# Kernel tuning notes

Hardware: AMD Instinct MI355X
Metric: run time of the kernel (lower is better)

## Reference

```python
import jax, jax.numpy as jnp
import numpy as np

EPS = 1e-06
SOUND_SPEED = 343.0
SUBBAND_EDGES = [500.0, 2000.0, 8000.0]
IS_SOUND_IDX = 0
RHO_IDX = 1
NUM_CANDIDATES = 64


def setup_inputs() -> dict:
    key = jax.random.key(0)
    ks = jax.random.split(key, 6)
    B, T, F, S, D = 16, 2048, 1025, 4, NUM_CANDIDATES
    phase = jax.random.normal(ks[0], (B, 1, T, F), dtype=jnp.float32)
    comb = jax.random.normal(ks[1], (B, 2, T, F), dtype=jnp.float32)
    scalar = jax.random.normal(ks[2], (B, T, S), dtype=jnp.float32)
    scalar_observed_mask = jax.random.uniform(ks[3], (B, T, S), dtype=jnp.float32)
    scalar_reliable_mask = jax.random.uniform(ks[4], (B, T, S), dtype=jnp.float32)
    stpacc = jax.random.normal(ks[5], (B, 1, T, D), dtype=jnp.float32)
    # STFT bin centers up to 24 kHz
    frequencies_hz = (jnp.arange(F, dtype=jnp.float32) * (24000.0 / (F - 1)))
    spacing_grid_hz = jnp.linspace(50.0, 1000.0, D, dtype=jnp.float32)
    return {
        'phase': phase, 'comb': comb, 'scalar': scalar,
        'scalar_observed_mask': scalar_observed_mask,
        'scalar_reliable_mask': scalar_reliable_mask,
        'stpacc': stpacc, 'frequencies_hz': frequencies_hz,
        'spacing_grid_hz': spacing_grid_hz,
    }


def _periodicity_basis(freq, spacing):
    # [D, F]: raised-cosine comb pattern for each candidate spacing
    pattern = 0.5 * (1.0 + jnp.cos(2.0 * np.pi * (freq[None, :] / jnp.maximum(spacing[:, None], 1e-06))))
    return pattern / jnp.maximum(pattern.mean(axis=-1, keepdims=True), EPS)


def _subband_masks(freq):
    # static boundaries: [min(f)] + edges + [max(f)+1]; all bands nonempty for this grid
    bounds = [jnp.min(freq)] + [jnp.float32(e) for e in SUBBAND_EDGES] + [jnp.max(freq) + 1.0]
    masks = [((freq >= lo) & (freq < hi)).astype(freq.dtype) for lo, hi in zip(bounds[:-1], bounds[1:])]
    return jnp.stack(masks, axis=0)  # [S_band, F]


def reference(phase, comb, scalar, scalar_observed_mask, scalar_reliable_mask,
              stpacc, frequencies_hz, spacing_grid_hz):
    freq = frequencies_hz.astype(phase.dtype)
    log_mag = phase[:, 0, :, :]                 # [B,T,F]
    smooth_d1 = comb[:, 0, :, :]
    abs_d1 = jnp.abs(comb[:, 1, :, :])
    log_mag_centered = log_mag - jnp.mean(log_mag, axis=-1, keepdims=True)
    trough = jax.nn.relu(-log_mag_centered)
    d1_strength = jax.nn.relu(abs_d1) + 0.25 * jax.nn.relu(jnp.abs(smooth_d1))
    trough = trough * (1.0 + d1_strength)
    trough = trough / jnp.maximum(jnp.mean(trough, axis=-1, keepdims=True), EPS)

    basis = _periodicity_basis(freq, spacing_grid_hz.astype(phase.dtype))  # [D,F]
    D, F = basis.shape
    periodic_score = jnp.einsum('btf,df->btd', trough, basis) / float(F)

    channels = [periodic_score]
    bands = _subband_masks(freq)                           # [Sb,F]
    denom = jnp.maximum(jnp.sum(bands, axis=-1), 1.0)      # [Sb]
    masked_basis = basis[None, :, :] * bands[:, None, :]   # [Sb,D,F]
    band_scores = jnp.einsum('btf,sdf->bstd', trough, masked_basis) / denom[None, :, None, None]
    channels += [band_scores[:, s] for s in range(bands.shape[0])]

    # stpacc projection (last dim already == D, no interpolation needed)
    stp = jax.nn.relu(stpacc[:, 0, :, :])
    stp = stp / jnp.maximum(jnp.mean(stp, axis=-1, keepdims=True), EPS)
    channels.append(stp)

    B, T = trough.shape[0], trough.shape[1]
    obs_quality = jnp.broadcast_to(jnp.mean(scalar_observed_mask, axis=-1, keepdims=True), (B, T, D))
    rel_quality = jnp.broadcast_to(jnp.mean(scalar_reliable_mask, axis=-1, keepdims=True), (B, T, D))
    channels.append(obs_quality)
    channels.append(rel_quality)

    is_sound = jnp.broadcast_to(jnp.clip(scalar[:, :, IS_SOUND_IDX:IS_SOUND_IDX + 1], 0.0, 1.0), (B, T, D))
    channels.append(is_sound)
    rho = jnp.broadcast_to(jnp.abs(jnp.clip(scalar[:, :, RHO_IDX:RHO_IDX + 1], -1.0, 1.0)), (B, T, D))
    channels.append(rho)

    raw_likelihood_seq = jnp.stack(channels, axis=-1)      # [B,T,D,10]
    raw_distance_logits_seq = jnp.mean(raw_likelihood_seq, axis=-1) * (0.5 + 0.5 * is_sound)

    distance_grid_cm = (100.0 * SOUND_SPEED) / (2.0 * jnp.maximum(spacing_grid_hz, 1e-06))
    return (raw_likelihood_seq, raw_distance_logits_seq,
            spacing_grid_hz.astype(phase.dtype), distance_grid_cm.astype(phase.dtype))
```

## Files before the change

### kernel.cpp

```cpp
#include <hip/hip_runtime.h>
#include <hip/hip_fp16.h>
#include <math.h>

#define Bn 16
#define Tn 2048
#define Fn 1025
#define KP 1056
#define KROW 1064
#define ROWS 16
#define NSLOT 11
#define Dn 64
#define EPSF 1e-6f

typedef __attribute__((ext_vector_type(8))) _Float16 f16x8;
typedef __attribute__((ext_vector_type(4))) _Float16 f16x4;
typedef __attribute__((ext_vector_type(4))) float f32x4;

__device__ inline float waveReduceSum(float v) {
#pragma unroll
  for (int off = 32; off > 0; off >>= 1) v += __shfl_xor(v, off, 64);
  return v;
}

__global__ __launch_bounds__(256) void prep_kernel(
    const float* __restrict__ freq, const float* __restrict__ spacing,
    _Float16* __restrict__ basisT, float* __restrict__ out2, float* __restrict__ out3) {
  __shared__ float wsum[4];
  const int d = blockIdx.x;
  const int tid = threadIdx.x;
  const float sp = fmaxf(spacing[d], 1e-6f);

  float pv[5];
  float lsum = 0.f;
#pragma unroll
  for (int it = 0; it < 5; ++it) {
    int f = tid + 256 * it;
    float p = 0.f;
    if (f < Fn) {
      double arg = 6.2831853071795864769 * (double)(freq[f] / sp);
      p = 0.5f * (1.0f + (float)cos(arg));
      lsum += p;
    }
    pv[it] = p;
  }
  float s = waveReduceSum(lsum);
  if ((tid & 63) == 0) wsum[tid >> 6] = s;
  __syncthreads();
  float inv = 1.0f / fmaxf((wsum[0] + wsum[1] + wsum[2] + wsum[3]) * (1.0f / 1025.0f), EPSF);

#pragma unroll
  for (int it = 0; it < 5; ++it) {
    int f = tid + 256 * it;
    if (f < KP) basisT[(size_t)d * KP + f] = (_Float16)(pv[it] * inv);
  }
  if (tid == 0) {
    out2[d] = spacing[d];
    out3[d] = 17150.0f / sp;
  }
}

__global__ __launch_bounds__(1024) void fused_kernel(
    const float* __restrict__ phase, const float* __restrict__ comb,
    const _Float16* __restrict__ basisT,
    const float* __restrict__ scalar, const float* __restrict__ obs_m,
    const float* __restrict__ rel_m, const float* __restrict__ stpacc,
    float* __restrict__ out0, float* __restrict__ out1) {
  __shared__ _Float16 uLDS[ROWS * KROW];
  __shared__ float cumS[ROWS * NSLOT * 65];
  __shared__ float rowScale[ROWS];

  const int lane = threadIdx.x & 63;
  const int w = __builtin_amdgcn_readfirstlane(threadIdx.x >> 6);
  const int row0 = blockIdx.x * ROWS;

  {
    const int row = row0 + w;
    const int b = row >> 11;
    const int t = row & 2047;
    const float* prow  = phase + (size_t)row * Fn;
    const float* c0row = comb + ((size_t)(b * 2 + 0) * Tn + t) * Fn;
    const float* c1row = comb + ((size_t)(b * 2 + 1) * Tn + t) * Fn;

    float4 pv[5], c0v[5], c1v[5];
#pragma unroll
    for (int it = 0; it < 5; ++it) {
      const int i = lane + 64 * it;
      if (i < 256) {
        pv[it]  = *(const float4*)(prow  + 4 * i);
        c0v[it] = *(const float4*)(c0row + 4 * i);
        c1v[it] = *(const float4*)(c1row + 4 * i);
      } else if (i == 256) {
        pv[it]  = make_float4(prow[1024],  0.f, 0.f, 0.f);
        c0v[it] = make_float4(c0row[1024], 0.f, 0.f, 0.f);
        c1v[it] = make_float4(c1row[1024], 0.f, 0.f, 0.f);
      } else {
        pv[it]  = make_float4(0.f, 0.f, 0.f, 0.f);
        c0v[it] = make_float4(0.f, 0.f, 0.f, 0.f);
        c1v[it] = make_float4(0.f, 0.f, 0.f, 0.f);
      }
    }

    float s = 0.f;
#pragma unroll
    for (int it = 0; it < 5; ++it)
      s += pv[it].x + pv[it].y + pv[it].z + pv[it].w;
    s = waveReduceSum(s);
    const float mean_lm = s * (1.0f / 1025.0f);

    _Float16* urow = uLDS + (size_t)w * KROW;
    float su = 0.f;
#pragma unroll
    for (int it = 0; it < 5; ++it) {
      const int i = lane + 64 * it;
      float4 u;
      const float* pf = (const float*)&pv[it];
      const float* q0 = (const float*)&c0v[it];
      const float* q1 = (const float*)&c1v[it];
      float* uf = (float*)&u;
#pragma unroll
      for (int c2 = 0; c2 < 4; ++c2) {
        float tr = fmaxf(mean_lm - pf[c2], 0.f);
        float d1 = fabsf(q1[c2]) + 0.25f * fabsf(q0[c2]);
        uf[c2] = tr * (1.f + d1);
      }
      if (i > 256) { u.x = 0.f; u.y = 0.f; u.z = 0.f; u.w = 0.f; }
      else if (i == 256) { u.y = 0.f; u.z = 0.f; u.w = 0.f; }
      su += u.x + u.y + u.z + u.w;
      if (i < 264) {
        f16x4 hv;
#pragma unroll
        for (int c2 = 0; c2 < 4; ++c2) hv[c2] = (_Float16)uf[c2];
        *(f16x4*)(urow + 4 * i) = hv;
      }
    }
    su = waveReduceSum(su);
    if (lane == 0) rowScale[w] = 1.0f / fmaxf(su * (1.0f / 1025.0f), EPSF);
  }
  __syncthreads();

  const int m16 = lane & 15;
  const int kg = lane >> 4;
  const int nh = w & 1;
  const int kh = w >> 1;
  const int d0 = nh * 32 + m16;

  const _Float16* ALp = uLDS + (size_t)m16 * KROW + kg * 8;
  const _Float16* B0 = basisT + (size_t)d0 * KP + kg * 8;
  const _Float16* B1 = basisT + (size_t)(d0 + 16) * KP + kg * 8;

  f32x4 acc0 = {0.f, 0.f, 0.f, 0.f};
  f32x4 acc1 = {0.f, 0.f, 0.f, 0.f};

  auto loadA = [&](int kt) { return *(const f16x8*)(ALp + kt * 32); };
  auto tileA = [&](int kt, f16x8 a) {
    f16x8 b0 = *(const f16x8*)(B0 + kt * 32);
    f16x8 b1 = *(const f16x8*)(B1 + kt * 32);
    acc0 = __builtin_amdgcn_mfma_f32_16x16x32_f16(a, b0, acc0, 0, 0, 0);
    acc1 = __builtin_amdgcn_mfma_f32_16x16x32_f16(a, b1, acc1, 0, 0, 0);
  };
  auto stor = [&](int slot, const f32x4& v0, const f32x4& v1) {
#pragma unroll
    for (int r = 0; r < 4; ++r) {
      const int rr = kg * 4 + r;
      cumS[(rr * NSLOT + slot) * 65 + d0]      = v0[r];
      cumS[(rr * NSLOT + slot) * 65 + d0 + 16] = v1[r];
    }
  };
  auto boundary = [&](int kt, int KB, f32x4& sa, f32x4& sb) {
    f16x8 a = loadA(kt);
    const int kb = kt * 32 + kg * 8;
    f16x8 alo, ahi;
#pragma unroll
    for (int j = 0; j < 8; ++j) {
      bool lo = (kb + j) < KB;
      alo[j] = lo ? a[j] : (_Float16)0.f;
      ahi[j] = lo ? (_Float16)0.f : a[j];
    }
    tileA(kt, alo);
    sa = acc0; sb = acc1;
    tileA(kt, ahi);
  };

  if (kh == 0) {
    f32x4 s0a = acc0, s0b = acc0, s1a = acc0, s1b = acc0;
    boundary(0, 22, s0a, s0b);
    tileA(1, loadA(1));
    boundary(2, 86, s1a, s1b);
    tileA(3, loadA(3));
    stor(0, acc0, acc1);
    stor(8, s0a, s0b);
    stor(9, s1a, s1b);
  } else if (kh == 2) {
    f32x4 s2a = acc0, s2b = acc0;
    tileA(8, loadA(8));
    tileA(9, loadA(9));
    boundary(10, 342, s2a, s2b);
    tileA(11, loadA(11));
    stor(2, acc0, acc1);
    stor(10, s2a, s2b);
  } else {
    const int kb = kh * 4;
    const int ke = (kh == 7) ? 33 : kb + 4;
#pragma unroll 4
    for (int kt = kb; kt < ke; ++kt) tileA(kt, loadA(kt));
    stor(kh, acc0, acc1);
  }
  __syncthreads();

  {
    const int rl = w;
    const size_t bt = (size_t)(row0 + rl);
    const float rs = rowScale[rl];

    float sv = fmaxf(stpacc[bt * Dn + lane], 0.f);

    float q[NSLOT];
#pragma unroll
    for (int s2 = 0; s2 < NSLOT; ++s2)
      q[s2] = cumS[(rl * NSLOT + s2) * 65 + lane];

    float total = q[0] + q[1] + q[2] + q[3] + q[4] + q[5] + q[6] + q[7];
    float cum342 = q[0] + q[1] + q[10];

    float ssum = waveReduceSum(sv);
    float stp = sv / fmaxf(ssum * (1.0f / 64.0f), EPSF);

    float4 scv = *(const float4*)(scalar + bt * 4);
    float4 om  = *(const float4*)(obs_m  + bt * 4);
    float4 rm  = *(const float4*)(rel_m  + bt * 4);
    float obs_q = (om.x + om.y + om.z + om.w) * 0.25f;
    float rel_q = (rm.x + rm.y + rm.z + rm.w) * 0.25f;
    float is_snd = fminf(fmaxf(scv.x, 0.f), 1.f);
    float rho = fabsf(fminf(fmaxf(scv.y, -1.f), 1.f));

    float c0 = total * rs * (1.0f / 1025.0f);
    float c1 = q[8] * rs * (1.0f / 22.0f);
    float c2 = (q[9] - q[8]) * rs * (1.0f / 64.0f);
    float c3 = (cum342 - q[9]) * rs * (1.0f / 256.0f);
    float c4 = (total - cum342) * rs * (1.0f / 683.0f);

    float mean10 = (c0 + c1 + c2 + c3 + c4 + stp + obs_q + rel_q + is_snd + rho) * 0.1f;
    float logit = mean10 * (0.5f + 0.5f * is_snd);

    float2* op = (float2*)(out0 + (bt * Dn + lane) * 10);
    op[0] = make_float2(c0, c1);
    op[1] = make_float2(c2, c3);
    op[2] = make_float2(c4, stp);
    op[3] = make_float2(obs_q, rel_q);
    op[4] = make_float2(is_snd, rho);
    out1[bt * Dn + lane] = logit;
  }
}

extern "C" void kernel_launch(void* const* d_in, const int* in_sizes, int n_in,
                              void* d_out, int out_size, void* d_ws, size_t ws_size,
                              hipStream_t stream) {
  const float* phase   = (const float*)d_in[0];
  const float* comb    = (const float*)d_in[1];
  const float* scalar  = (const float*)d_in[2];
  const float* obs_m   = (const float*)d_in[3];
  const float* rel_m   = (const float*)d_in[4];
  const float* stpacc  = (const float*)d_in[5];
  const float* freq    = (const float*)d_in[6];
  const float* spacing = (const float*)d_in[7];

  float* out  = (float*)d_out;
  float* out0 = out;
  float* out1 = out + (size_t)Bn * Tn * Dn * 10;
  float* out2 = out1 + (size_t)Bn * Tn * Dn;
  float* out3 = out2 + Dn;

  _Float16* basisT = (_Float16*)d_ws;

  prep_kernel<<<Dn, 256, 0, stream>>>(freq, spacing, basisT, out2, out3);
  fused_kernel<<<Bn * Tn / ROWS, 1024, 0, stream>>>(
      phase, comb, basisT, scalar, obs_m, rel_m, stpacc, out0, out1);
}
```

Measured before the change: 137.4 us.

## Halve fused kernel block to 512 threads with two rows per wave

The fused kernel now launches 8 waves per block instead of 16. Each wave processes two rows in the load/transform and epilogue phases. The MFMA K-split is regrouped into four K-quarters with 8 tiles each, which cuts partial-sum slots from 11 to 7 and shrinks the cumS LDS footprint. The aim is fewer partial sums and less LDS per block, allowing more resident blocks. The cost is more serial work per wave, and the row loads now run sequentially inside a loop that is not unrolled.

```diff
diff --git a/kernel.cpp b/kernel.cpp
--- a/kernel.cpp
+++ b/kernel.cpp
@@ -8,7 +8,7 @@
 #define KP 1056
 #define KROW 1064
 #define ROWS 16
-#define NSLOT 11
+#define NSLOT 7
 #define Dn 64
 #define EPSF 1e-6f
 
@@ -59,7 +59,7 @@
   }
 }
 
-__global__ __launch_bounds__(1024) void fused_kernel(
+__global__ __launch_bounds__(512) void fused_kernel(
     const float* __restrict__ phase, const float* __restrict__ comb,
     const _Float16* __restrict__ basisT,
     const float* __restrict__ scalar, const float* __restrict__ obs_m,
@@ -73,8 +73,10 @@
   const int w = __builtin_amdgcn_readfirstlane(threadIdx.x >> 6);
   const int row0 = blockIdx.x * ROWS;
 
-  {
-    const int row = row0 + w;
+#pragma unroll 1
+  for (int k2 = 0; k2 < 2; ++k2) {
+    const int rl = 2 * w + k2;
+    const int row = row0 + rl;
     const int b = row >> 11;
     const int t = row & 2047;
     const float* prow  = phase + (size_t)row * Fn;
@@ -107,7 +109,7 @@
     s = waveReduceSum(s);
     const float mean_lm = s * (1.0f / 1025.0f);
 
-    _Float16* urow = uLDS + (size_t)w * KROW;
+    _Float16* urow = uLDS + (size_t)rl * KROW;
     float su = 0.f;
 #pragma unroll
     for (int it = 0; it < 5; ++it) {
@@ -134,14 +136,14 @@
       }
     }
     su = waveReduceSum(su);
-    if (lane == 0) rowScale[w] = 1.0f / fmaxf(su * (1.0f / 1025.0f), EPSF);
+    if (lane == 0) rowScale[rl] = 1.0f / fmaxf(su * (1.0f / 1025.0f), EPSF);
   }
   __syncthreads();
 
   const int m16 = lane & 15;
   const int kg = lane >> 4;
   const int nh = w & 1;
-  const int kh = w >> 1;
+  const int kq = w >> 1;
   const int d0 = nh * 32 + m16;
 
   const _Float16* ALp = uLDS + (size_t)m16 * KROW + kg * 8;
@@ -181,34 +183,41 @@
     tileA(kt, ahi);
   };
 
-  if (kh == 0) {
-    f32x4 s0a = acc0, s0b = acc0, s1a = acc0, s1b = acc0;
-    boundary(0, 22, s0a, s0b);
+  if (kq == 0) {
+    f32x4 za = {0.f, 0.f, 0.f, 0.f};
+    f32x4 s22a = za, s22b = za, s86a = za, s86b = za;
+    boundary(0, 22, s22a, s22b);
     tileA(1, loadA(1));
-    boundary(2, 86, s1a, s1b);
-    tileA(3, loadA(3));
+    boundary(2, 86, s86a, s86b);
+#pragma unroll
+    for (int kt = 3; kt < 8; ++kt) tileA(kt, loadA(kt));
     stor(0, acc0, acc1);
-    stor(8, s0a, s0b);
-    stor(9, s1a, s1b);
-  } else if (kh == 2) {
-    f32x4 s2a = acc0, s2b = acc0;
+    stor(4, s22a, s22b);
+    stor(5, s86a, s86b);
+  } else if (kq == 1) {
+    f32x4 za = {0.f, 0.f, 0.f, 0.f};
+    f32x4 s342a = za, s342b = za;
     tileA(8, loadA(8));
     tileA(9, loadA(9));
-    boundary(10, 342, s2a, s2b);
-    tileA(11, loadA(11));
+    boundary(10, 342, s342a, s342b);
+#pragma unroll
+    for (int kt = 11; kt < 17; ++kt) tileA(kt, loadA(kt));
+    stor(1, acc0, acc1);
+    stor(6, s342a, s342b);
+  } else if (kq == 2) {
+#pragma unroll
+    for (int kt = 17; kt < 25; ++kt) tileA(kt, loadA(kt));
     stor(2, acc0, acc1);
-    stor(10, s2a, s2b);
   } else {
-    const int kb = kh * 4;
-    const int ke = (kh == 7) ? 33 : kb + 4;
-#pragma unroll 4
-    for (int kt = kb; kt < ke; ++kt) tileA(kt, loadA(kt));
-    stor(kh, acc0, acc1);
+#pragma unroll
+    for (int kt = 25; kt < 33; ++kt) tileA(kt, loadA(kt));
+    stor(3, acc0, acc1);
   }
   __syncthreads();
 
-  {
-    const int rl = w;
+#pragma unroll
+  for (int k2 = 0; k2 < 2; ++k2) {
+    const int rl = 2 * w + k2;
     const size_t bt = (size_t)(row0 + rl);
     const float rs = rowScale[rl];
 
@@ -219,8 +228,8 @@
     for (int s2 = 0; s2 < NSLOT; ++s2)
       q[s2] = cumS[(rl * NSLOT + s2) * 65 + lane];
 
-    float total = q[0] + q[1] + q[2] + q[3] + q[4] + q[5] + q[6] + q[7];
-    float cum342 = q[0] + q[1] + q[10];
+    float total = q[0] + q[1] + q[2] + q[3];
+    float cum342 = q[0] + q[6];
 
     float ssum = waveReduceSum(sv);
     float stp = sv / fmaxf(ssum * (1.0f / 64.0f), EPSF);
@@ -234,9 +243,9 @@
     float rho = fabsf(fminf(fmaxf(scv.y, -1.f), 1.f));
 
     float c0 = total * rs * (1.0f / 1025.0f);
-    float c1 = q[8] * rs * (1.0f / 22.0f);
-    float c2 = (q[9] - q[8]) * rs * (1.0f / 64.0f);
-    float c3 = (cum342 - q[9]) * rs * (1.0f / 256.0f);
+    float c1 = q[4] * rs * (1.0f / 22.0f);
+    float c2 = (q[5] - q[4]) * rs * (1.0f / 64.0f);
+    float c3 = (cum342 - q[5]) * rs * (1.0f / 256.0f);
     float c4 = (total - cum342) * rs * (1.0f / 683.0f);
 
     float mean10 = (c0 + c1 + c2 + c3 + c4 + stp + obs_q + rel_q + is_snd + rho) * 0.1f;
@@ -273,6 +282,6 @@
   _Float16* basisT = (_Float16*)d_ws;
 
   prep_kernel<<<Dn, 256, 0, stream>>>(freq, spacing, basisT, out2, out3);
-  fused_kernel<<<Bn * Tn / ROWS, 1024, 0, stream>>>(
+  fused_kernel<<<Bn * Tn / ROWS, 512, 0, stream>>>(
       phase, comb, basisT, scalar, obs_m, rel_m, stpacc, out0, out1);
 }
```

Measured after the change: 118.5 us, median of 2. 1.16x faster.
